# Optimization experiments

Measured on AMD Instinct MI355X. Metric: run time of the kernel, lower is better.

Reference implementation:

```python
import jax, jax.numpy as jnp
import numpy as np

S = 4      # num_residual_streams
I = 1      # num_branch_inputs
DIM = 2048
LAYER_INDEX = 0


def setup_inputs() -> dict:
    key = jax.random.key(0)
    ks = jax.random.split(key, 6)
    residuals = jax.random.normal(ks[0], (16, 2048, DIM), dtype=jnp.float32)
    # RMSNorm weight (init 1.0, small noise for non-trivial math)
    norm_weight = 1.0 + 0.02 * jax.random.normal(ks[1], (DIM,), dtype=jnp.float32)
    # static_beta: ones[S, I]
    static_beta = jnp.ones((S, I), dtype=jnp.float32) + 0.02 * jax.random.normal(ks[2], (S, I), dtype=jnp.float32)
    # static_alpha: cat([alpha0 (one-hot row at layer_index), eye(S)], dim=1) -> [S, I+S]
    alpha0 = jnp.zeros((S, I), dtype=jnp.float32).at[LAYER_INDEX, :].set(1.0)
    static_alpha = jnp.concatenate([alpha0, jnp.eye(S, dtype=jnp.float32)], axis=1)
    dynamic_alpha_fn = 0.02 * jax.random.normal(ks[3], (DIM, S + I), dtype=jnp.float32)
    dynamic_alpha_scale = jnp.float32(0.01)
    dynamic_beta_fn = 0.02 * jax.random.normal(ks[4], (DIM, I), dtype=jnp.float32)
    dynamic_beta_scale = jnp.float32(0.01)
    return dict(residuals=residuals, norm_weight=norm_weight, static_alpha=static_alpha,
                static_beta=static_beta, dynamic_alpha_fn=dynamic_alpha_fn,
                dynamic_alpha_scale=dynamic_alpha_scale, dynamic_beta_fn=dynamic_beta_fn,
                dynamic_beta_scale=dynamic_beta_scale)


def reference(residuals, norm_weight, static_alpha, static_beta,
              dynamic_alpha_fn, dynamic_alpha_scale, dynamic_beta_fn, dynamic_beta_scale):
    bs, L, D = residuals.shape
    b = bs // S
    # '(b s) l d -> b l s d'  (stream index is the inner factor of the leading axis)
    x = residuals.reshape(b, S, L, D).transpose(0, 2, 1, 3)  # [b, L, S, D]

    # RMSNorm over last dim (torch default eps = finfo.eps)
    eps = jnp.finfo(x.dtype).eps
    normed = x * jax.lax.rsqrt(jnp.mean(x * x, axis=-1, keepdims=True) + eps) * norm_weight

    # width connection
    alpha = jnp.tanh(normed @ dynamic_alpha_fn) * dynamic_alpha_scale + static_alpha  # [b,L,S,S+I]
    beta = jnp.tanh(normed @ dynamic_beta_fn) * dynamic_beta_scale + static_beta      # [b,L,S,I]
    mix_h = jnp.einsum('blst,blsd->bltd', alpha, x)                                   # [b,L,S+I,D]

    branch_input = mix_h[..., :I, :]   # [b,L,I,D]
    res = mix_h[..., I:, :]            # [b,L,S,D]

    # branch is identity; 'b l i d -> i b l d'
    branch_out = branch_input.transpose(2, 0, 1, 3)  # [I,b,L,D]

    # depth connection
    res = jnp.einsum('ibld,blsi->blsd', branch_out, beta) + res  # [b,L,S,D]
    # 'b l s d -> (b s) l d'
    out = res.transpose(0, 2, 1, 3).reshape(b * S, L, D)
    return out
```

## Files before the change

kernel.cpp:

```cpp
#include <hip/hip_runtime.h>


#define DD 2048
#define NS 4
#define NT 5

__global__ void prep_kernel(const float* __restrict__ w,
                            const float* __restrict__ A,
                            const float* __restrict__ Bfn,
                            float* __restrict__ WA,
                            float* __restrict__ WB) {
    int d = blockIdx.x * blockDim.x + threadIdx.x;
    if (d >= DD) return;
    float wf = w[d];
#pragma unroll
    for (int t = 0; t < NT; ++t)
        WA[t * DD + d] = wf * A[d * NT + t];
    WB[d] = wf * Bfn[d];
}

#define DOT4(ACC, V) do { \
    ACC = fmaf(xv.x, (V).x, ACC); \
    ACC = fmaf(xv.y, (V).y, ACC); \
    ACC = fmaf(xv.z, (V).z, ACC); \
    ACC = fmaf(xv.w, (V).w, ACC); \
} while (0)

#define ACC4(O, V, C) do { \
    O.x = fmaf((C), (V).x, O.x); \
    O.y = fmaf((C), (V).y, O.y); \
    O.z = fmaf((C), (V).z, O.z); \
    O.w = fmaf((C), (V).w, O.w); \
} while (0)

__global__ __launch_bounds__(256) void hyper_kernel(
    const float* __restrict__ X,
    const float* __restrict__ WA,
    const float* __restrict__ WB,
    const float* __restrict__ sA,
    const float* __restrict__ sB,
    const float* __restrict__ aS,
    const float* __restrict__ bS,
    float* __restrict__ out)
{
    __shared__ __align__(16) float xs[NS][DD];
    __shared__ float shA[NS][NT];

    const int g  = blockIdx.x;
    const int bb = g >> 11;
    const int l  = g & 2047;
    const int wv = threadIdx.x >> 6;
    const int ln = threadIdx.x & 63;

    const size_t rowOff = (((size_t)(bb * NS + wv)) * 2048 + (size_t)l) * (size_t)DD;

    float a0 = 0.f, a1 = 0.f, a2 = 0.f, a3 = 0.f, a4 = 0.f, ab = 0.f, ss = 0.f;

#pragma unroll
    for (int it = 0; it < 8; ++it) {
        const int d0 = it * 256 + ln * 4;
        const float4 xv = *(const float4*)(X + rowOff + d0);
        *(float4*)&xs[wv][d0] = xv;
        ss = fmaf(xv.x, xv.x, ss);
        ss = fmaf(xv.y, xv.y, ss);
        ss = fmaf(xv.z, xv.z, ss);
        ss = fmaf(xv.w, xv.w, ss);

        const float4 w0 = *(const float4*)(WA + 0 * DD + d0);
        const float4 w1 = *(const float4*)(WA + 1 * DD + d0);
        const float4 w2 = *(const float4*)(WA + 2 * DD + d0);
        const float4 w3 = *(const float4*)(WA + 3 * DD + d0);
        const float4 w4 = *(const float4*)(WA + 4 * DD + d0);
        const float4 wb = *(const float4*)(WB + d0);
        DOT4(a0, w0); DOT4(a1, w1); DOT4(a2, w2);
        DOT4(a3, w3); DOT4(a4, w4); DOT4(ab, wb);
    }

#pragma unroll
    for (int m = 1; m < 64; m <<= 1) {
        a0 += __shfl_xor(a0, m);
        a1 += __shfl_xor(a1, m);
        a2 += __shfl_xor(a2, m);
        a3 += __shfl_xor(a3, m);
        a4 += __shfl_xor(a4, m);
        ab += __shfl_xor(ab, m);
        ss += __shfl_xor(ss, m);
    }

    const float rms = rsqrtf(ss * (1.0f / 2048.0f) + 1.1920929e-07f);
    const float asc = aS[0];
    const float bsc = bS[0];
    const float be  = tanhf(rms * ab) * bsc + sB[wv];
    if (ln == 0) {
        shA[wv][0] = tanhf(rms * a0) * asc + sA[wv * NT + 0];
        shA[wv][1] = tanhf(rms * a1) * asc + sA[wv * NT + 1];
        shA[wv][2] = tanhf(rms * a2) * asc + sA[wv * NT + 2];
        shA[wv][3] = tanhf(rms * a3) * asc + sA[wv * NT + 3];
        shA[wv][4] = tanhf(rms * a4) * asc + sA[wv * NT + 4];
    }
    __syncthreads();

    const float c0 = shA[0][wv + 1] + be * shA[0][0];
    const float c1 = shA[1][wv + 1] + be * shA[1][0];
    const float c2 = shA[2][wv + 1] + be * shA[2][0];
    const float c3 = shA[3][wv + 1] + be * shA[3][0];

#pragma unroll
    for (int it = 0; it < 8; ++it) {
        const int d0 = it * 256 + ln * 4;
        const float4 v0 = *(const float4*)&xs[0][d0];
        const float4 v1 = *(const float4*)&xs[1][d0];
        const float4 v2 = *(const float4*)&xs[2][d0];
        const float4 v3 = *(const float4*)&xs[3][d0];
        float4 o = make_float4(0.f, 0.f, 0.f, 0.f);
        ACC4(o, v0, c0); ACC4(o, v1, c1); ACC4(o, v2, c2); ACC4(o, v3, c3);
        *(float4*)(out + rowOff + d0) = o;
    }
}

extern "C" void kernel_launch(void* const* d_in, const int* in_sizes, int n_in,
                              void* d_out, int out_size, void* d_ws, size_t ws_size,
                              hipStream_t stream) {
    const float* X   = (const float*)d_in[0];
    const float* w   = (const float*)d_in[1];
    const float* sA  = (const float*)d_in[2];
    const float* sB  = (const float*)d_in[3];
    const float* Afn = (const float*)d_in[4];
    const float* aSc = (const float*)d_in[5];
    const float* Bfn = (const float*)d_in[6];
    const float* bSc = (const float*)d_in[7];
    float* out = (float*)d_out;

    float* WA = (float*)d_ws;
    float* WB = WA + 5 * 2048;

    prep_kernel<<<8, 256, 0, stream>>>(w, Afn, Bfn, WA, WB);
    hyper_kernel<<<4 * 2048, 256, 0, stream>>>(X, WA, WB, sA, sB, aSc, bSc, out);
}
```

Measured before the change: 489.7 us.

## Keep all four stream rows in registers and drop the LDS staging

Restructures the kernel so each thread holds one float4 slice from all four residual streams in registers, instead of having each wave own one stream and stage it through shared memory. Per-stream partial dot products are reduced across waves through a small shared array, and the coefficients are broadcast with lane shuffles. Blocks grow to 512 threads with a 6-blocks-per-CU bound, and outputs use nontemporal stores. This removes the 32KB shared-memory tile, which should raise occupancy. In exchange, the register count and the shuffle work per thread both go up (28 values reduced instead of 7).

```diff
diff --git a/kernel.cpp b/kernel.cpp
--- a/kernel.cpp
+++ b/kernel.cpp
@@ -4,6 +4,10 @@
 #define DD 2048
 #define NS 4
 #define NT 5
+#define NW 8
+#define ROWSTRIDE ((size_t)DD * 2048)
+
+typedef float v4f __attribute__((ext_vector_type(4)));
 
 __global__ void prep_kernel(const float* __restrict__ w,
                             const float* __restrict__ A,
@@ -19,21 +23,11 @@
     WB[d] = wf * Bfn[d];
 }
 
-#define DOT4(ACC, V) do { \
-    ACC = fmaf(xv.x, (V).x, ACC); \
-    ACC = fmaf(xv.y, (V).y, ACC); \
-    ACC = fmaf(xv.z, (V).z, ACC); \
-    ACC = fmaf(xv.w, (V).w, ACC); \
-} while (0)
+__device__ __forceinline__ float dot4(v4f a, v4f b) {
+    return fmaf(a.x, b.x, fmaf(a.y, b.y, fmaf(a.z, b.z, a.w * b.w)));
+}
 
-#define ACC4(O, V, C) do { \
-    O.x = fmaf((C), (V).x, O.x); \
-    O.y = fmaf((C), (V).y, O.y); \
-    O.z = fmaf((C), (V).z, O.z); \
-    O.w = fmaf((C), (V).w, O.w); \
-} while (0)
-
-__global__ __launch_bounds__(256) void hyper_kernel(
+__global__ __launch_bounds__(512, 6) void hyper_kernel(
     const float* __restrict__ X,
     const float* __restrict__ WA,
     const float* __restrict__ WB,
@@ -43,78 +37,90 @@
     const float* __restrict__ bS,
     float* __restrict__ out)
 {
-    __shared__ __align__(16) float xs[NS][DD];
-    __shared__ float shA[NS][NT];
+    __shared__ float shP[NW][NS][7];
 
     const int g  = blockIdx.x;
     const int bb = g >> 11;
     const int l  = g & 2047;
     const int wv = threadIdx.x >> 6;
     const int ln = threadIdx.x & 63;
+    const int d0 = (wv << 8) + (ln << 2);
 
-    const size_t rowOff = (((size_t)(bb * NS + wv)) * 2048 + (size_t)l) * (size_t)DD;
+    const size_t base = ((size_t)(bb * NS) * 2048 + (size_t)l) * (size_t)DD + (size_t)d0;
 
-    float a0 = 0.f, a1 = 0.f, a2 = 0.f, a3 = 0.f, a4 = 0.f, ab = 0.f, ss = 0.f;
+    v4f xv[NS];
+#pragma unroll
+    for (int s = 0; s < NS; ++s)
+        xv[s] = *(const v4f*)(X + base + (size_t)s * ROWSTRIDE);
 
+    v4f wt[6];
 #pragma unroll
-    for (int it = 0; it < 8; ++it) {
-        const int d0 = it * 256 + ln * 4;
-        const float4 xv = *(const float4*)(X + rowOff + d0);
-        *(float4*)&xs[wv][d0] = xv;
-        ss = fmaf(xv.x, xv.x, ss);
-        ss = fmaf(xv.y, xv.y, ss);
-        ss = fmaf(xv.z, xv.z, ss);
-        ss = fmaf(xv.w, xv.w, ss);
+    for (int t = 0; t < NT; ++t)
+        wt[t] = *(const v4f*)(WA + t * DD + d0);
+    wt[5] = *(const v4f*)(WB + d0);
 
-        const float4 w0 = *(const float4*)(WA + 0 * DD + d0);
-        const float4 w1 = *(const float4*)(WA + 1 * DD + d0);
-        const float4 w2 = *(const float4*)(WA + 2 * DD + d0);
-        const float4 w3 = *(const float4*)(WA + 3 * DD + d0);
-        const float4 w4 = *(const float4*)(WA + 4 * DD + d0);
-        const float4 wb = *(const float4*)(WB + d0);
-        DOT4(a0, w0); DOT4(a1, w1); DOT4(a2, w2);
-        DOT4(a3, w3); DOT4(a4, w4); DOT4(ab, wb);
+    float acc[NS][7];
+#pragma unroll
+    for (int s = 0; s < NS; ++s) {
+#pragma unroll
+        for (int t = 0; t < 6; ++t)
+            acc[s][t] = dot4(xv[s], wt[t]);
+        acc[s][6] = dot4(xv[s], xv[s]);
     }
 
 #pragma unroll
     for (int m = 1; m < 64; m <<= 1) {
-        a0 += __shfl_xor(a0, m);
-        a1 += __shfl_xor(a1, m);
-        a2 += __shfl_xor(a2, m);
-        a3 += __shfl_xor(a3, m);
-        a4 += __shfl_xor(a4, m);
-        ab += __shfl_xor(ab, m);
-        ss += __shfl_xor(ss, m);
+#pragma unroll
+        for (int s = 0; s < NS; ++s)
+#pragma unroll
+            for (int k = 0; k < 7; ++k)
+                acc[s][k] += __shfl_xor(acc[s][k], m);
     }
 
-    const float rms = rsqrtf(ss * (1.0f / 2048.0f) + 1.1920929e-07f);
-    const float asc = aS[0];
-    const float bsc = bS[0];
-    const float be  = tanhf(rms * ab) * bsc + sB[wv];
     if (ln == 0) {
-        shA[wv][0] = tanhf(rms * a0) * asc + sA[wv * NT + 0];
-        shA[wv][1] = tanhf(rms * a1) * asc + sA[wv * NT + 1];
-        shA[wv][2] = tanhf(rms * a2) * asc + sA[wv * NT + 2];
-        shA[wv][3] = tanhf(rms * a3) * asc + sA[wv * NT + 3];
-        shA[wv][4] = tanhf(rms * a4) * asc + sA[wv * NT + 4];
+#pragma unroll
+        for (int s = 0; s < NS; ++s)
+#pragma unroll
+            for (int k = 0; k < 7; ++k)
+                shP[wv][s][k] = acc[s][k];
     }
     __syncthreads();
 
-    const float c0 = shA[0][wv + 1] + be * shA[0][0];
-    const float c1 = shA[1][wv + 1] + be * shA[1][0];
-    const float c2 = shA[2][wv + 1] + be * shA[2][0];
-    const float c3 = shA[3][wv + 1] + be * shA[3][0];
+    const float ascale = aS[0];
+    const float bscale = bS[0];
+    float val = 0.f;
+    if (ln < 24) {
+        const bool isA = ln < 20;
+        const int s   = isA ? (ln / 5) : (ln - 20);
+        const int idx = isA ? (ln % 5) : 5;
+        float dv = 0.f, sv = 0.f;
+#pragma unroll
+        for (int w = 0; w < NW; ++w) {
+            dv += shP[w][s][idx];
+            sv += shP[w][s][6];
+        }
+        const float rms = rsqrtf(sv * (1.0f / 2048.0f) + 1.1920929e-07f);
+        const float th  = tanhf(rms * dv);
+        val = isA ? fmaf(th, ascale, sA[ln]) : fmaf(th, bscale, sB[s]);
+    }
+
+    float bet[NS];
+#pragma unroll
+    for (int s = 0; s < NS; ++s) bet[s] = __shfl(val, 20 + s);
+
+    float c[NS][NS];
+#pragma unroll
+    for (int sp = 0; sp < NS; ++sp) {
+        const float a0 = __shfl(val, sp * 5);
+#pragma unroll
+        for (int s = 0; s < NS; ++s)
+            c[s][sp] = fmaf(bet[s], a0, __shfl(val, sp * 5 + s + 1));
+    }
 
 #pragma unroll
-    for (int it = 0; it < 8; ++it) {
-        const int d0 = it * 256 + ln * 4;
-        const float4 v0 = *(const float4*)&xs[0][d0];
-        const float4 v1 = *(const float4*)&xs[1][d0];
-        const float4 v2 = *(const float4*)&xs[2][d0];
-        const float4 v3 = *(const float4*)&xs[3][d0];
-        float4 o = make_float4(0.f, 0.f, 0.f, 0.f);
-        ACC4(o, v0, c0); ACC4(o, v1, c1); ACC4(o, v2, c2); ACC4(o, v3, c3);
-        *(float4*)(out + rowOff + d0) = o;
+    for (int s = 0; s < NS; ++s) {
+        v4f o = c[s][0] * xv[0] + c[s][1] * xv[1] + c[s][2] * xv[2] + c[s][3] * xv[3];
+        __builtin_nontemporal_store(o, (v4f*)(out + base + (size_t)s * ROWSTRIDE));
     }
 }
 
@@ -135,5 +141,5 @@
     float* WB = WA + 5 * 2048;
 
     prep_kernel<<<8, 256, 0, stream>>>(w, Afn, Bfn, WA, WB);
-    hyper_kernel<<<4 * 2048, 256, 0, stream>>>(X, WA, WB, sA, sB, aSc, bSc, out);
+    hyper_kernel<<<4 * 2048, 512, 0, stream>>>(X, WA, WB, sA, sB, aSc, bSc, out);
 }
```

New measurement: 489.8 us. Within noise of the previous version (+0.0%).
